# Kernel tuning notes

Measured on AMD Instinct MI355X. Metric: run time of the kernel, lower is better.

Reference implementation:

```python
import jax, jax.numpy as jnp
import numpy as np

USER = 100000
ITEM = 50000
N = USER + ITEM          # total nodes in bipartite graph
LAT = 64                 # args.latdim
TXT = 768                # args.text_feat_dim
E = 2400000              # nnz per sparse adjacency
GNN_LAYERS = 2           # args.gnn_layer
RIS_LAMBDA = 0.2         # args.ris_adj_lambda


def setup_inputs() -> dict:
    key = jax.random.key(0)
    ks = jax.random.split(key, 11)
    return {
        "uEmbeds": jax.random.normal(ks[0], (USER, LAT), jnp.float32) * 0.1,
        "iEmbeds": jax.random.normal(ks[1], (ITEM, LAT), jnp.float32) * 0.1,
        "text_embedding": jax.random.normal(ks[2], (ITEM, TXT), jnp.float32),
        "W_text": jax.random.normal(ks[3], (TXT, LAT), jnp.float32) * (1.0 / np.sqrt(TXT)),
        "b_text": jnp.zeros((LAT,), jnp.float32),
        "adj_vals": jax.random.uniform(ks[4], (E,), jnp.float32) / 16.0,
        "t_vals": jax.random.uniform(ks[5], (E,), jnp.float32) / 16.0,
        "adj_rows": jax.random.randint(ks[6], (E,), 0, N, jnp.int32),
        "adj_cols": jax.random.randint(ks[7], (E,), 0, N, jnp.int32),
        "t_rows": jax.random.randint(ks[8], (E,), 0, N, jnp.int32),
        "t_cols": jax.random.randint(ks[9], (E,), 0, N, jnp.int32),
    }


def _spmm(rows, cols, vals, x, n):
    # out[r] = sum_{e: rows[e]==r} vals[e] * x[cols[e]]  (torch.spmm on COO)
    return jax.ops.segment_sum(vals[:, None] * x[cols], rows, num_segments=n)


def _l2_normalize(x, eps=1e-12):
    # F.normalize(x, p=2, dim=1)
    nrm = jnp.sqrt(jnp.sum(x * x, axis=1, keepdims=True))
    return x / jnp.maximum(nrm, eps)


def reference(uEmbeds, iEmbeds, text_embedding, W_text, b_text,
              adj_vals, t_vals, adj_rows, adj_cols, t_rows, t_cols):
    # trans == 1: Linear projection of text features
    text_feats = text_embedding @ W_text + b_text                      # [ITEM, LAT]

    # self-propagation through text adjacency
    embeds_ta = _spmm(t_rows, t_cols, t_vals,
                      jnp.concatenate([uEmbeds, iEmbeds], axis=0), N)  # [N, LAT]

    # first hop: users + normalized text feats
    e1 = _spmm(adj_rows, adj_cols, adj_vals,
               jnp.concatenate([uEmbeds, _l2_normalize(text_feats)], axis=0), N)

    # second hop: aggregated users + raw item embeds
    e2 = _spmm(adj_rows, adj_cols, adj_vals,
               jnp.concatenate([e1[:USER], iEmbeds], axis=0), N)

    embeds = e1 + e2 + RIS_LAMBDA * embeds_ta

    # stacked GCN layers, sum of all layer outputs (incl. layer 0)
    total = embeds
    cur = embeds
    for _ in range(GNN_LAYERS):
        cur = _spmm(adj_rows, adj_cols, adj_vals, cur, N)
        total = total + cur

    return total[:USER], total[USER:]
```

## Files before the change

### kernel.cpp

```cpp
#include <hip/hip_runtime.h>

#define USER  100000
#define ITEM  50000
#define NNODE 150000
#define LAT   64
#define TXT   768
#define RP    150016
#define NBUCK 8
#define BROWS (NNODE / NBUCK)
#define SCHUNK 4096
#define CAP   64
#define GEMMB 782

typedef unsigned long long u64;

__device__ __forceinline__ void gemm_body(
    float (*As)[68], float (*Bs)[64],
    const float* __restrict__ text, const float* __restrict__ W,
    const float* __restrict__ b, float* __restrict__ tf,
    int nitems, int blk)
{
    const int tid = threadIdx.x;
    const int tx  = tid & 15;
    const int ty  = tid >> 4;
    const int row0 = blk * 64;

    float acc[4][4] = {};

    const int lrow = tid >> 3;
    const int lk4  = (tid & 7) * 4;

    for (int k0 = 0; k0 < TXT; k0 += 32) {
#pragma unroll
        for (int half = 0; half < 2; ++half) {
            int r = lrow + half * 32;
            int gr = row0 + r;
            if (gr >= nitems) gr = nitems - 1;
            float4 tv = *(const float4*)(text + (size_t)gr * TXT + k0 + lk4);
            As[lk4 + 0][r] = tv.x;
            As[lk4 + 1][r] = tv.y;
            As[lk4 + 2][r] = tv.z;
            As[lk4 + 3][r] = tv.w;
        }
        const float4* wf = (const float4*)(W + (size_t)k0 * LAT);
        ((float4*)Bs)[tid]       = wf[tid];
        ((float4*)Bs)[tid + 256] = wf[tid + 256];
        __syncthreads();

#pragma unroll
        for (int k = 0; k < 32; ++k) {
            float4 a4 = *(const float4*)&As[k][ty * 4];
            float4 b4 = *(const float4*)&Bs[k][tx * 4];
            float av[4] = {a4.x, a4.y, a4.z, a4.w};
            float bv[4] = {b4.x, b4.y, b4.z, b4.w};
#pragma unroll
            for (int i = 0; i < 4; ++i)
#pragma unroll
                for (int j = 0; j < 4; ++j)
                    acc[i][j] = fmaf(av[i], bv[j], acc[i][j]);
        }
        __syncthreads();
    }

    float4 b4 = *(const float4*)(b + tx * 4);
    float bv[4] = {b4.x, b4.y, b4.z, b4.w};
#pragma unroll
    for (int i = 0; i < 4; ++i) {
        float v[4];
        float ss = 0.f;
#pragma unroll
        for (int j = 0; j < 4; ++j) {
            v[j] = acc[i][j] + bv[j];
            ss = fmaf(v[j], v[j], ss);
        }
        ss += __shfl_xor(ss, 1);
        ss += __shfl_xor(ss, 2);
        ss += __shfl_xor(ss, 4);
        ss += __shfl_xor(ss, 8);
        float inv = 1.0f / fmaxf(sqrtf(ss), 1e-12f);
        int gr = row0 + ty * 4 + i;
        if (gr < nitems) {
            float4 o = {v[0] * inv, v[1] * inv, v[2] * inv, v[3] * inv};
            *(float4*)(tf + (size_t)gr * LAT + tx * 4) = o;
        }
    }
}

__device__ __forceinline__ void scatter_body(
    const int* __restrict__ rows, const int* __restrict__ cols,
    const float* __restrict__ vals, int* __restrict__ fil,
    u64* __restrict__ epk, int n, int bucket, int chunk)
{
    const int lo = bucket * BROWS;
    const int hi = lo + BROWS;
    const int base = chunk * SCHUNK + threadIdx.x;

    int  r[16];
    bool m[16];
    u64  pk[16];
    int  pos[16];

#pragma unroll
    for (int i = 0; i < 16; ++i) {
        int e = base + i * 256;
        bool inb = e < n;
        int rr = inb ? rows[e] : -1;
        r[i] = rr;
        m[i] = inb && (rr >= lo) && (rr < hi);
    }
#pragma unroll
    for (int i = 0; i < 16; ++i) {
        int e = base + i * 256;
        if (m[i])
            pk[i] = ((u64)__float_as_uint(vals[e]) << 32) | (unsigned)cols[e];
    }
#pragma unroll
    for (int i = 0; i < 16; ++i)
        if (m[i]) pos[i] = atomicAdd(&fil[r[i]], 1);
#pragma unroll
    for (int i = 0; i < 16; ++i)
        if (m[i] && pos[i] < CAP)
            epk[((size_t)r[i] << 6) + pos[i]] = pk[i];
}

__global__ __launch_bounds__(256) void mega1_kernel(
    const float* __restrict__ text, const float* __restrict__ W,
    const float* __restrict__ b, float* __restrict__ tf, int nitems,
    const int* __restrict__ arows, const int* __restrict__ acols,
    const float* __restrict__ avals, int* __restrict__ filA, u64* __restrict__ epkA,
    const int* __restrict__ trows, const int* __restrict__ tcols,
    const float* __restrict__ tvals, int* __restrict__ filT, u64* __restrict__ epkT,
    int nedges, int nchunk, int nscat)
{
    __shared__ float As[32][68];
    __shared__ float Bs[32][64];

    const int bid = blockIdx.x;
    const int gi  = bid / 72;
    const int pos = bid % 72;

    if (pos < 64) {
        const int so = gi * 64 + pos;
        if (so >= nscat) return;
        const int bucket = so & 7;
        const int cm     = so >> 3;
        if (cm < nchunk)
            scatter_body(arows, acols, avals, filA, epkA, nedges, bucket, cm);
        else
            scatter_body(trows, tcols, tvals, filT, epkT, nedges, bucket, cm - nchunk);
    } else {
        const int go = gi * 8 + (pos - 64);
        if (go < GEMMB)
            gemm_body(As, Bs, text, W, b, tf, nitems, go);
    }
}

__global__ __launch_bounds__(256) void gemm_norm_kernel(
    const float* __restrict__ text, const float* __restrict__ W,
    const float* __restrict__ b, float* __restrict__ tf, int nitems)
{
    __shared__ float As[32][68];
    __shared__ float Bs[32][64];
    gemm_body(As, Bs, text, W, b, tf, nitems, blockIdx.x);
}

__device__ __forceinline__ void spmm_row(
    int r, int lane, const int* __restrict__ cnt, const u64* __restrict__ epk,
    const float* __restrict__ xu, const float* __restrict__ xi,
    float scale, const float* __restrict__ add1, const float* __restrict__ add2,
    float* __restrict__ out, float* __restrict__ out2, int out2_assign)
{
    const int g = lane >> 4;
    const int l = lane & 15;

    const u64* rowp = epk + ((size_t)r << 6);
    const int deg = min(cnt[r], CAP);

    float4 acc = {0.f, 0.f, 0.f, 0.f};

    u64 pk[4];
#pragma unroll
    for (int i = 0; i < 4; ++i) pk[i] = rowp[g + i * 4];
#pragma unroll
    for (int i = 0; i < 4; ++i) {
        int ee = g + i * 4;
        if (ee < deg) {
            int   c = (int)(unsigned)(pk[i] & 0xffffffffu);
            float v = __uint_as_float((unsigned)(pk[i] >> 32));
            const float* x = (c < USER) ? (xu + (size_t)c * LAT)
                                        : (xi + (size_t)(c - USER) * LAT);
            float4 xv = *(const float4*)(x + 4 * l);
            acc.x = fmaf(v, xv.x, acc.x);
            acc.y = fmaf(v, xv.y, acc.y);
            acc.z = fmaf(v, xv.z, acc.z);
            acc.w = fmaf(v, xv.w, acc.w);
        }
    }

    if (deg > 16) {
        u64 pk2[4];
#pragma unroll
        for (int i = 0; i < 4; ++i) pk2[i] = rowp[16 + g + i * 4];
#pragma unroll
        for (int i = 0; i < 4; ++i) {
            int ee = 16 + g + i * 4;
            if (ee < deg) {
                int   c = (int)(unsigned)(pk2[i] & 0xffffffffu);
                float v = __uint_as_float((unsigned)(pk2[i] >> 32));
                const float* x = (c < USER) ? (xu + (size_t)c * LAT)
                                            : (xi + (size_t)(c - USER) * LAT);
                float4 xv = *(const float4*)(x + 4 * l);
                acc.x = fmaf(v, xv.x, acc.x);
                acc.y = fmaf(v, xv.y, acc.y);
                acc.z = fmaf(v, xv.z, acc.z);
                acc.w = fmaf(v, xv.w, acc.w);
            }
        }
        for (int ee = 32 + g; ee < deg; ee += 4) {
            u64 p = rowp[ee];
            int   c = (int)(unsigned)(p & 0xffffffffu);
            float v = __uint_as_float((unsigned)(p >> 32));
            const float* x = (c < USER) ? (xu + (size_t)c * LAT)
                                        : (xi + (size_t)(c - USER) * LAT);
            float4 xv = *(const float4*)(x + 4 * l);
            acc.x = fmaf(v, xv.x, acc.x);
            acc.y = fmaf(v, xv.y, acc.y);
            acc.z = fmaf(v, xv.z, acc.z);
            acc.w = fmaf(v, xv.w, acc.w);
        }
    }

#pragma unroll
    for (int off = 16; off <= 32; off <<= 1) {
        acc.x += __shfl_xor(acc.x, off);
        acc.y += __shfl_xor(acc.y, off);
        acc.z += __shfl_xor(acc.z, off);
        acc.w += __shfl_xor(acc.w, off);
    }
    if (g == 0) {
        size_t idx = (size_t)r * LAT + 4 * l;
        float4 res = {scale * acc.x, scale * acc.y, scale * acc.z, scale * acc.w};
        if (add1) {
            float4 a = *(const float4*)(add1 + idx);
            res.x += a.x; res.y += a.y; res.z += a.z; res.w += a.w;
        }
        if (add2) {
            float4 a = *(const float4*)(add2 + idx);
            res.x += a.x; res.y += a.y; res.z += a.z; res.w += a.w;
        }
        if (out) *(float4*)(out + idx) = res;
        if (out2) {
            if (out2_assign) {
                *(float4*)(out2 + idx) = res;
            } else {
                float4 o = *(const float4*)(out2 + idx);
                o.x += res.x; o.y += res.y; o.z += res.z; o.w += res.w;
                *(float4*)(out2 + idx) = o;
            }
        }
    }
}

__global__ __launch_bounds__(256) void spmm_kernel(
    const int* __restrict__ cnt, const u64* __restrict__ epk,
    const float* __restrict__ xu, const float* __restrict__ xi,
    float scale, const float* __restrict__ add1, const float* __restrict__ add2,
    float* __restrict__ out, float* __restrict__ out2, int out2_assign, int n)
{
    int r = blockIdx.x * 4 + (threadIdx.x >> 6);
    if (r >= n) return;
    spmm_row(r, threadIdx.x & 63, cnt, epk, xu, xi, scale,
             add1, add2, out, out2, out2_assign);
}

__global__ __launch_bounds__(256) void spmm_pair_kernel(
    const int* __restrict__ cnt0, const u64* __restrict__ epk0,
    const float* __restrict__ xu0, const float* __restrict__ xi0,
    float s0, float* __restrict__ out0,
    const int* __restrict__ cnt1, const u64* __restrict__ epk1,
    const float* __restrict__ xu1, const float* __restrict__ xi1,
    float s1, float* __restrict__ out1, int n)
{
    int m  = blockIdx.x & 1;
    int r  = (blockIdx.x >> 1) * 4 + (threadIdx.x >> 6);
    if (r >= n) return;
    int lane = threadIdx.x & 63;
    if (m == 0)
        spmm_row(r, lane, cnt0, epk0, xu0, xi0, s0, nullptr, nullptr,
                 out0, nullptr, 0);
    else
        spmm_row(r, lane, cnt1, epk1, xu1, xi1, s1, nullptr, nullptr,
                 out1, nullptr, 0);
}

__global__ __launch_bounds__(256) void spmm_atomic_kernel(
    const int* __restrict__ rows, const int* __restrict__ cols,
    const float* __restrict__ vals, float scale,
    const float* __restrict__ xu, const float* __restrict__ xi,
    float* __restrict__ out, int nedges)
{
    int e = blockIdx.x * 4 + (threadIdx.x >> 6);
    if (e >= nedges) return;
    int lane = threadIdx.x & 63;
    int r = rows[e];
    int c = cols[e];
    float v = vals[e] * scale;
    const float* x = (c < USER) ? (xu + (size_t)c * LAT)
                                : (xi + (size_t)(c - USER) * LAT);
    atomicAdd(&out[(size_t)r * LAT + lane], v * x[lane]);
}

__global__ __launch_bounds__(256) void combine_kernel(
    float* __restrict__ A, const float* __restrict__ B,
    float* __restrict__ out, int n4)
{
    int i = blockIdx.x * blockDim.x + threadIdx.x;
    if (i >= n4) return;
    float4 a = ((const float4*)A)[i];
    float4 b = ((const float4*)B)[i];
    a.x += b.x; a.y += b.y; a.z += b.z; a.w += b.w;
    ((float4*)A)[i]   = a;
    ((float4*)out)[i] = a;
}

__global__ __launch_bounds__(256) void add_kernel(
    float* __restrict__ out, const float* __restrict__ src, int n4)
{
    int i = blockIdx.x * blockDim.x + threadIdx.x;
    if (i >= n4) return;
    float4 o = ((const float4*)out)[i];
    float4 s = ((const float4*)src)[i];
    o.x += s.x; o.y += s.y; o.z += s.z; o.w += s.w;
    ((float4*)out)[i] = o;
}

extern "C" void kernel_launch(void* const* d_in, const int* in_sizes, int n_in,
                              void* d_out, int out_size, void* d_ws, size_t ws_size,
                              hipStream_t stream)
{
    const float* u        = (const float*)d_in[0];
    const float* it       = (const float*)d_in[1];
    const float* text     = (const float*)d_in[2];
    const float* W        = (const float*)d_in[3];
    const float* b        = (const float*)d_in[4];
    const float* adj_vals = (const float*)d_in[5];
    const float* t_vals   = (const float*)d_in[6];
    const int*   adj_rows = (const int*)d_in[7];
    const int*   adj_cols = (const int*)d_in[8];
    const int*   t_rows   = (const int*)d_in[9];
    const int*   t_cols   = (const int*)d_in[10];
    const int E = in_sizes[5];

    float* out = (float*)d_out;

    char* p = (char*)d_ws;
    size_t used = 0;
    auto carve = [&](size_t bytes) {
        char* q = p + used;
        used += (bytes + 255) & ~(size_t)255;
        return q;
    };
    float* A    = (float*)carve((size_t)NNODE * LAT * 4);
    float* B    = (float*)carve((size_t)NNODE * LAT * 4);
    float* tf   = (float*)carve((size_t)ITEM * LAT * 4);
    int*   filA = (int*)  carve((size_t)RP * 4);
    int*   filT = (int*)  carve((size_t)RP * 4);
    u64*   epkA = (u64*)  carve((size_t)NNODE * CAP * 8);
    u64*   epkT = (u64*)  carve((size_t)NNODE * CAP * 8);
    bool padded = (used <= ws_size);

    const int sblk   = (NNODE + 3) / 4;
    const int nchunk = (E + SCHUNK - 1) / SCHUNK;
    const int nscat  = 2 * nchunk * NBUCK;
    const int ngrp   = (nscat + 63) / 64;
    const int n4     = NNODE * LAT / 4;
    const int cblk   = (n4 + 255) / 256;

    if (padded) {
        hipMemsetAsync(filA, 0, (size_t)RP * 4 * 2, stream);
        mega1_kernel<<<ngrp * 72, 256, 0, stream>>>(
            text, W, b, tf, ITEM,
            adj_rows, adj_cols, adj_vals, filA, epkA,
            t_rows, t_cols, t_vals, filT, epkT, E, nchunk, nscat);

        spmm_pair_kernel<<<sblk * 2, 256, 0, stream>>>(
            filT, epkT, u, it, 0.2f, A,
            filA, epkA, u, tf, 1.0f, B, NNODE);

        spmm_kernel<<<sblk, 256, 0, stream>>>(filA, epkA, B, it, 1.0f,
                                              A, B, A, nullptr, 0, NNODE);
        spmm_kernel<<<sblk, 256, 0, stream>>>(filA, epkA,
                                              A, A + (size_t)USER * LAT, 1.0f,
                                              nullptr, nullptr, B, nullptr, 0, NNODE);
        spmm_kernel<<<sblk, 256, 0, stream>>>(filA, epkA,
                                              B, B + (size_t)USER * LAT, 1.0f,
                                              A, B, out, nullptr, 0, NNODE);
        return;
    }

    const size_t nbuf = (size_t)NNODE * LAT * 4;
    const int ablk = (E + 3) / 4;
    const int gblk = (ITEM + 63) / 64;
    gemm_norm_kernel<<<gblk, 256, 0, stream>>>(text, W, b, tf, ITEM);
    hipMemsetAsync(A, 0, nbuf, stream);
    hipMemsetAsync(B, 0, nbuf, stream);
    spmm_atomic_kernel<<<ablk, 256, 0, stream>>>(t_rows, t_cols, t_vals, 0.2f,
                                                 u, it, A, E);
    spmm_atomic_kernel<<<ablk, 256, 0, stream>>>(adj_rows, adj_cols, adj_vals, 1.0f,
                                                 u, tf, B, E);
    spmm_atomic_kernel<<<ablk, 256, 0, stream>>>(adj_rows, adj_cols, adj_vals, 1.0f,
                                                 B, it, A, E);
    combine_kernel<<<cblk, 256, 0, stream>>>(A, B, out, n4);
    hipMemsetAsync(B, 0, nbuf, stream);
    spmm_atomic_kernel<<<ablk, 256, 0, stream>>>(adj_rows, adj_cols, adj_vals, 1.0f,
                                                 A, A + (size_t)USER * LAT, B, E);
    add_kernel<<<cblk, 256, 0, stream>>>(out, B, n4);
    hipMemsetAsync(A, 0, nbuf, stream);
    spmm_atomic_kernel<<<ablk, 256, 0, stream>>>(adj_rows, adj_cols, adj_vals, 1.0f,
                                                 B, B + (size_t)USER * LAT, A, E);
    add_kernel<<<cblk, 256, 0, stream>>>(out, A, n4);
}
```

Baseline: 704.2 us.

## Gather SpMM operands from fp16 copies to halve random-gather traffic

Converts the user/item embeddings and the normalized text features to fp16, and has each SpMM pass also write an fp16 copy of its output for the next hop. The gathers in the CSR-bucket SpMM then read 8 bytes per lane instead of 16, while accumulation and the fp32 outputs are kept. The fp16 conversion of the inputs is folded into spare blocks of the fused scatter/GEMM kernel, and the A16 buffer reuses the epkT region once the text adjacency is consumed. The cost is reduced precision in the propagated activations, a workspace layout change, and a fallback chain if the workspace is too small.

After: 647.9 us. 8.0% less time.

```diff
diff --git a/kernel.cpp b/kernel.cpp
--- a/kernel.cpp
+++ b/kernel.cpp
@@ -1,4 +1,5 @@
 #include <hip/hip_runtime.h>
+#include <hip/hip_fp16.h>
 
 #define USER  100000
 #define ITEM  50000
@@ -14,10 +15,32 @@
 
 typedef unsigned long long u64;
 
+__device__ __forceinline__ void store4(float* p, float4 v) { *(float4*)p = v; }
+__device__ __forceinline__ void store4(__half* p, float4 v)
+{
+    __half2* d = (__half2*)p;
+    d[0] = __floats2half2_rn(v.x, v.y);
+    d[1] = __floats2half2_rn(v.z, v.w);
+}
+__device__ __forceinline__ float4 load_x4(const float* x, int l)
+{
+    return *(const float4*)(x + 4 * l);
+}
+__device__ __forceinline__ float4 load_x4(const __half* x, int l)
+{
+    float2 raw = *(const float2*)(x + 4 * l);
+    __half2 h0 = *reinterpret_cast<const __half2*>(&raw.x);
+    __half2 h1 = *reinterpret_cast<const __half2*>(&raw.y);
+    float2 f0 = __half22float2(h0);
+    float2 f1 = __half22float2(h1);
+    return make_float4(f0.x, f0.y, f1.x, f1.y);
+}
+
+template<typename TFT>
 __device__ __forceinline__ void gemm_body(
     float (*As)[68], float (*Bs)[64],
     const float* __restrict__ text, const float* __restrict__ W,
-    const float* __restrict__ b, float* __restrict__ tf,
+    const float* __restrict__ b, TFT* __restrict__ tf,
     int nitems, int blk)
 {
     const int tid = threadIdx.x;
@@ -79,10 +102,9 @@
         ss += __shfl_xor(ss, 8);
         float inv = 1.0f / fmaxf(sqrtf(ss), 1e-12f);
         int gr = row0 + ty * 4 + i;
-        if (gr < nitems) {
-            float4 o = {v[0] * inv, v[1] * inv, v[2] * inv, v[3] * inv};
-            *(float4*)(tf + (size_t)gr * LAT + tx * 4) = o;
-        }
+        if (gr < nitems)
+            store4(tf + (size_t)gr * LAT + tx * 4,
+                   make_float4(v[0] * inv, v[1] * inv, v[2] * inv, v[3] * inv));
     }
 }
 
@@ -123,14 +145,39 @@
             epk[((size_t)r[i] << 6) + pos[i]] = pk[i];
 }
 
+__device__ __forceinline__ void cvt_body(
+    const float* __restrict__ u, const float* __restrict__ it,
+    __half* __restrict__ u16, __half* __restrict__ it16,
+    int slot, int nslots)
+{
+    const long NG  = (long)NNODE * LAT / 8;
+    const long UG  = (long)USER * LAT / 8;
+    const long stride = (long)nslots * 256;
+    for (long g = (long)slot * 256 + threadIdx.x; g < NG; g += stride) {
+        const float* s; __half* d; long off;
+        if (g < UG) { s = u;  d = u16;  off = g * 8; }
+        else        { s = it; d = it16; off = (g - UG) * 8; }
+        const float4* s4 = (const float4*)(s + off);
+        float4 a = s4[0], c = s4[1];
+        __half2* d2 = (__half2*)(d + off);
+        d2[0] = __floats2half2_rn(a.x, a.y);
+        d2[1] = __floats2half2_rn(a.z, a.w);
+        d2[2] = __floats2half2_rn(c.x, c.y);
+        d2[3] = __floats2half2_rn(c.z, c.w);
+    }
+}
+
+template<typename TFT>
 __global__ __launch_bounds__(256) void mega1_kernel(
     const float* __restrict__ text, const float* __restrict__ W,
-    const float* __restrict__ b, float* __restrict__ tf, int nitems,
+    const float* __restrict__ b, TFT* __restrict__ tf, int nitems,
     const int* __restrict__ arows, const int* __restrict__ acols,
     const float* __restrict__ avals, int* __restrict__ filA, u64* __restrict__ epkA,
     const int* __restrict__ trows, const int* __restrict__ tcols,
     const float* __restrict__ tvals, int* __restrict__ filT, u64* __restrict__ epkT,
-    int nedges, int nchunk, int nscat)
+    int nedges, int nchunk, int nscat,
+    const float* __restrict__ u, const float* __restrict__ it,
+    __half* __restrict__ u16, __half* __restrict__ it16, int ncvt)
 {
     __shared__ float As[32][68];
     __shared__ float Bs[32][64];
@@ -151,7 +198,9 @@
     } else {
         const int go = gi * 8 + (pos - 64);
         if (go < GEMMB)
-            gemm_body(As, Bs, text, W, b, tf, nitems, go);
+            gemm_body<TFT>(As, Bs, text, W, b, tf, nitems, go);
+        else if (u16 && go - GEMMB < ncvt)
+            cvt_body(u, it, u16, it16, go - GEMMB, ncvt);
     }
 }
 
@@ -161,14 +210,15 @@
 {
     __shared__ float As[32][68];
     __shared__ float Bs[32][64];
-    gemm_body(As, Bs, text, W, b, tf, nitems, blockIdx.x);
-}
-
+    gemm_body<float>(As, Bs, text, W, b, tf, nitems, blockIdx.x);
+}
+
+template<typename XT>
 __device__ __forceinline__ void spmm_row(
     int r, int lane, const int* __restrict__ cnt, const u64* __restrict__ epk,
-    const float* __restrict__ xu, const float* __restrict__ xi,
+    const XT* __restrict__ xu, const XT* __restrict__ xi,
     float scale, const float* __restrict__ add1, const float* __restrict__ add2,
-    float* __restrict__ out, float* __restrict__ out2, int out2_assign)
+    float* __restrict__ out32, __half* __restrict__ out16)
 {
     const int g = lane >> 4;
     const int l = lane & 15;
@@ -187,9 +237,9 @@
         if (ee < deg) {
             int   c = (int)(unsigned)(pk[i] & 0xffffffffu);
             float v = __uint_as_float((unsigned)(pk[i] >> 32));
-            const float* x = (c < USER) ? (xu + (size_t)c * LAT)
-                                        : (xi + (size_t)(c - USER) * LAT);
-            float4 xv = *(const float4*)(x + 4 * l);
+            const XT* x = (c < USER) ? (xu + (size_t)c * LAT)
+                                     : (xi + (size_t)(c - USER) * LAT);
+            float4 xv = load_x4(x, l);
             acc.x = fmaf(v, xv.x, acc.x);
             acc.y = fmaf(v, xv.y, acc.y);
             acc.z = fmaf(v, xv.z, acc.z);
@@ -207,9 +257,9 @@
             if (ee < deg) {
                 int   c = (int)(unsigned)(pk2[i] & 0xffffffffu);
                 float v = __uint_as_float((unsigned)(pk2[i] >> 32));
-                const float* x = (c < USER) ? (xu + (size_t)c * LAT)
-                                            : (xi + (size_t)(c - USER) * LAT);
-                float4 xv = *(const float4*)(x + 4 * l);
+                const XT* x = (c < USER) ? (xu + (size_t)c * LAT)
+                                         : (xi + (size_t)(c - USER) * LAT);
+                float4 xv = load_x4(x, l);
                 acc.x = fmaf(v, xv.x, acc.x);
                 acc.y = fmaf(v, xv.y, acc.y);
                 acc.z = fmaf(v, xv.z, acc.z);
@@ -220,9 +270,9 @@
             u64 p = rowp[ee];
             int   c = (int)(unsigned)(p & 0xffffffffu);
             float v = __uint_as_float((unsigned)(p >> 32));
-            const float* x = (c < USER) ? (xu + (size_t)c * LAT)
-                                        : (xi + (size_t)(c - USER) * LAT);
-            float4 xv = *(const float4*)(x + 4 * l);
+            const XT* x = (c < USER) ? (xu + (size_t)c * LAT)
+                                     : (xi + (size_t)(c - USER) * LAT);
+            float4 xv = load_x4(x, l);
             acc.x = fmaf(v, xv.x, acc.x);
             acc.y = fmaf(v, xv.y, acc.y);
             acc.z = fmaf(v, xv.z, acc.z);
@@ -248,49 +298,43 @@
             float4 a = *(const float4*)(add2 + idx);
             res.x += a.x; res.y += a.y; res.z += a.z; res.w += a.w;
         }
-        if (out) *(float4*)(out + idx) = res;
-        if (out2) {
-            if (out2_assign) {
-                *(float4*)(out2 + idx) = res;
-            } else {
-                float4 o = *(const float4*)(out2 + idx);
-                o.x += res.x; o.y += res.y; o.z += res.z; o.w += res.w;
-                *(float4*)(out2 + idx) = o;
-            }
-        }
-    }
-}
-
+        *(float4*)(out32 + idx) = res;
+        if (out16) store4(out16 + idx, res);
+    }
+}
+
+template<typename XT>
 __global__ __launch_bounds__(256) void spmm_kernel(
     const int* __restrict__ cnt, const u64* __restrict__ epk,
-    const float* __restrict__ xu, const float* __restrict__ xi,
+    const XT* __restrict__ xu, const XT* __restrict__ xi,
     float scale, const float* __restrict__ add1, const float* __restrict__ add2,
-    float* __restrict__ out, float* __restrict__ out2, int out2_assign, int n)
+    float* __restrict__ out32, __half* __restrict__ out16, int n)
 {
     int r = blockIdx.x * 4 + (threadIdx.x >> 6);
     if (r >= n) return;
-    spmm_row(r, threadIdx.x & 63, cnt, epk, xu, xi, scale,
-             add1, add2, out, out2, out2_assign);
-}
-
+    spmm_row<XT>(r, threadIdx.x & 63, cnt, epk, xu, xi, scale,
+                 add1, add2, out32, out16);
+}
+
+template<typename XT>
 __global__ __launch_bounds__(256) void spmm_pair_kernel(
     const int* __restrict__ cnt0, const u64* __restrict__ epk0,
-    const float* __restrict__ xu0, const float* __restrict__ xi0,
-    float s0, float* __restrict__ out0,
+    const XT* __restrict__ xu0, const XT* __restrict__ xi0,
+    float s0, float* __restrict__ out0, __half* __restrict__ o16_0,
     const int* __restrict__ cnt1, const u64* __restrict__ epk1,
-    const float* __restrict__ xu1, const float* __restrict__ xi1,
-    float s1, float* __restrict__ out1, int n)
+    const XT* __restrict__ xu1, const XT* __restrict__ xi1,
+    float s1, float* __restrict__ out1, __half* __restrict__ o16_1, int n)
 {
     int m  = blockIdx.x & 1;
     int r  = (blockIdx.x >> 1) * 4 + (threadIdx.x >> 6);
     if (r >= n) return;
     int lane = threadIdx.x & 63;
     if (m == 0)
-        spmm_row(r, lane, cnt0, epk0, xu0, xi0, s0, nullptr, nullptr,
-                 out0, nullptr, 0);
+        spmm_row<XT>(r, lane, cnt0, epk0, xu0, xi0, s0, nullptr, nullptr,
+                     out0, o16_0);
     else
-        spmm_row(r, lane, cnt1, epk1, xu1, xi1, s1, nullptr, nullptr,
-                 out1, nullptr, 0);
+        spmm_row<XT>(r, lane, cnt1, epk1, xu1, xi1, s1, nullptr, nullptr,
+                     out1, o16_1);
 }
 
 __global__ __launch_bounds__(256) void spmm_atomic_kernel(
@@ -353,6 +397,14 @@
 
     float* out = (float*)d_out;
 
+    const int sblk   = (NNODE + 3) / 4;
+    const int nchunk = (E + SCHUNK - 1) / SCHUNK;
+    const int nscat  = 2 * nchunk * NBUCK;
+    const int ngrp   = (nscat + 63) / 64;
+    const int ncvt   = ngrp * 8 - GEMMB;
+    const int n4     = NNODE * LAT / 4;
+    const int cblk   = (n4 + 255) / 256;
+
     char* p = (char*)d_ws;
     size_t used = 0;
     auto carve = [&](size_t bytes) {
@@ -360,63 +412,98 @@
         used += (bytes + 255) & ~(size_t)255;
         return q;
     };
-    float* A    = (float*)carve((size_t)NNODE * LAT * 4);
-    float* B    = (float*)carve((size_t)NNODE * LAT * 4);
-    float* tf   = (float*)carve((size_t)ITEM * LAT * 4);
-    int*   filA = (int*)  carve((size_t)RP * 4);
-    int*   filT = (int*)  carve((size_t)RP * 4);
-    u64*   epkA = (u64*)  carve((size_t)NNODE * CAP * 8);
-    u64*   epkT = (u64*)  carve((size_t)NNODE * CAP * 8);
-    bool padded = (used <= ws_size);
-
-    const int sblk   = (NNODE + 3) / 4;
-    const int nchunk = (E + SCHUNK - 1) / SCHUNK;
-    const int nscat  = 2 * nchunk * NBUCK;
-    const int ngrp   = (nscat + 63) / 64;
-    const int n4     = NNODE * LAT / 4;
-    const int cblk   = (n4 + 255) / 256;
-
-    if (padded) {
+
+    used = 0;
+    float*  A    = (float*) carve((size_t)NNODE * LAT * 4);
+    float*  B    = (float*) carve((size_t)NNODE * LAT * 4);
+    int*    filA = (int*)   carve((size_t)RP * 4);
+    int*    filT = (int*)   carve((size_t)RP * 4);
+    u64*    epkA = (u64*)   carve((size_t)E ? (size_t)NNODE * CAP * 8 : 0);
+    u64*    epkT = (u64*)   carve((size_t)NNODE * CAP * 8);
+    __half* tf16 = (__half*)carve((size_t)ITEM * LAT * 2);
+    __half* u16  = (__half*)carve((size_t)NNODE * LAT * 2);
+    __half* it16 = u16 + (size_t)USER * LAT;
+    __half* B16  = (__half*)carve((size_t)NNODE * LAT * 2);
+    __half* A16  = (__half*)epkT;
+
+    if (used <= ws_size && ncvt > 0) {
         hipMemsetAsync(filA, 0, (size_t)RP * 4 * 2, stream);
-        mega1_kernel<<<ngrp * 72, 256, 0, stream>>>(
-            text, W, b, tf, ITEM,
+        mega1_kernel<__half><<<ngrp * 72, 256, 0, stream>>>(
+            text, W, b, tf16, ITEM,
             adj_rows, adj_cols, adj_vals, filA, epkA,
-            t_rows, t_cols, t_vals, filT, epkT, E, nchunk, nscat);
-
-        spmm_pair_kernel<<<sblk * 2, 256, 0, stream>>>(
-            filT, epkT, u, it, 0.2f, A,
-            filA, epkA, u, tf, 1.0f, B, NNODE);
-
-        spmm_kernel<<<sblk, 256, 0, stream>>>(filA, epkA, B, it, 1.0f,
-                                              A, B, A, nullptr, 0, NNODE);
-        spmm_kernel<<<sblk, 256, 0, stream>>>(filA, epkA,
-                                              A, A + (size_t)USER * LAT, 1.0f,
-                                              nullptr, nullptr, B, nullptr, 0, NNODE);
-        spmm_kernel<<<sblk, 256, 0, stream>>>(filA, epkA,
-                                              B, B + (size_t)USER * LAT, 1.0f,
-                                              A, B, out, nullptr, 0, NNODE);
+            t_rows, t_cols, t_vals, filT, epkT, E, nchunk, nscat,
+            u, it, u16, it16, ncvt);
+
+        spmm_pair_kernel<__half><<<sblk * 2, 256, 0, stream>>>(
+            filT, epkT, u16, it16, 0.2f, A, nullptr,
+            filA, epkA, u16, tf16, 1.0f, B, B16, NNODE);
+
+        spmm_kernel<__half><<<sblk, 256, 0, stream>>>(
+            filA, epkA, B16, it16, 1.0f, A, B, A, A16, NNODE);
+        spmm_kernel<__half><<<sblk, 256, 0, stream>>>(
+            filA, epkA, A16, A16 + (size_t)USER * LAT, 1.0f,
+            nullptr, nullptr, B, B16, NNODE);
+        spmm_kernel<__half><<<sblk, 256, 0, stream>>>(
+            filA, epkA, B16, B16 + (size_t)USER * LAT, 1.0f,
+            A, B, out, nullptr, NNODE);
         return;
     }
 
+    used = 0;
+    float* A2    = (float*)carve((size_t)NNODE * LAT * 4);
+    float* B2    = (float*)carve((size_t)NNODE * LAT * 4);
+    float* tf2   = (float*)carve((size_t)ITEM * LAT * 4);
+    int*   filA2 = (int*)  carve((size_t)RP * 4);
+    int*   filT2 = (int*)  carve((size_t)RP * 4);
+    u64*   epkA2 = (u64*)  carve((size_t)NNODE * CAP * 8);
+    u64*   epkT2 = (u64*)  carve((size_t)NNODE * CAP * 8);
+
+    if (used <= ws_size) {
+        hipMemsetAsync(filA2, 0, (size_t)RP * 4 * 2, stream);
+        mega1_kernel<float><<<ngrp * 72, 256, 0, stream>>>(
+            text, W, b, tf2, ITEM,
+            adj_rows, adj_cols, adj_vals, filA2, epkA2,
+            t_rows, t_cols, t_vals, filT2, epkT2, E, nchunk, nscat,
+            u, it, nullptr, nullptr, 0);
+
+        spmm_pair_kernel<float><<<sblk * 2, 256, 0, stream>>>(
+            filT2, epkT2, u, it, 0.2f, A2, nullptr,
+            filA2, epkA2, u, tf2, 1.0f, B2, nullptr, NNODE);
+
+        spmm_kernel<float><<<sblk, 256, 0, stream>>>(
+            filA2, epkA2, B2, it, 1.0f, A2, B2, A2, nullptr, NNODE);
+        spmm_kernel<float><<<sblk, 256, 0, stream>>>(
+            filA2, epkA2, A2, A2 + (size_t)USER * LAT, 1.0f,
+            nullptr, nullptr, B2, nullptr, NNODE);
+        spmm_kernel<float><<<sblk, 256, 0, stream>>>(
+            filA2, epkA2, B2, B2 + (size_t)USER * LAT, 1.0f,
+            A2, B2, out, nullptr, NNODE);
+        return;
+    }
+
+    used = 0;
+    float* A3  = (float*)carve((size_t)NNODE * LAT * 4);
+    float* B3  = (float*)carve((size_t)NNODE * LAT * 4);
+    float* tf3 = (float*)carve((size_t)ITEM * LAT * 4);
     const size_t nbuf = (size_t)NNODE * LAT * 4;
     const int ablk = (E + 3) / 4;
     const int gblk = (ITEM + 63) / 64;
-    gemm_norm_kernel<<<gblk, 256, 0, stream>>>(text, W, b, tf, ITEM);
-    hipMemsetAsync(A, 0, nbuf, stream);
-    hipMemsetAsync(B, 0, nbuf, stream);
+    gemm_norm_kernel<<<gblk, 256, 0, stream>>>(text, W, b, tf3, ITEM);
+    hipMemsetAsync(A3, 0, nbuf, stream);
+    hipMemsetAsync(B3, 0, nbuf, stream);
     spmm_atomic_kernel<<<ablk, 256, 0, stream>>>(t_rows, t_cols, t_vals, 0.2f,
-                                                 u, it, A, E);
+                                                 u, it, A3, E);
     spmm_atomic_kernel<<<ablk, 256, 0, stream>>>(adj_rows, adj_cols, adj_vals, 1.0f,
-                                                 u, tf, B, E);
+                                                 u, tf3, B3, E);
     spmm_atomic_kernel<<<ablk, 256, 0, stream>>>(adj_rows, adj_cols, adj_vals, 1.0f,
-                                                 B, it, A, E);
-    combine_kernel<<<cblk, 256, 0, stream>>>(A, B, out, n4);
-    hipMemsetAsync(B, 0, nbuf, stream);
+                                                 B3, it, A3, E);
+    combine_kernel<<<cblk, 256, 0, stream>>>(A3, B3, out, n4);
+    hipMemsetAsync(B3, 0, nbuf, stream);
     spmm_atomic_kernel<<<ablk, 256, 0, stream>>>(adj_rows, adj_cols, adj_vals, 1.0f,
-                                                 A, A + (size_t)USER * LAT, B, E);
-    add_kernel<<<cblk, 256, 0, stream>>>(out, B, n4);
-    hipMemsetAsync(A, 0, nbuf, stream);
+                                                 A3, A3 + (size_t)USER * LAT, B3, E);
+    add_kernel<<<cblk, 256, 0, stream>>>(out, B3, n4);
+    hipMemsetAsync(A3, 0, nbuf, stream);
     spmm_atomic_kernel<<<ablk, 256, 0, stream>>>(adj_rows, adj_cols, adj_vals, 1.0f,
-                                                 B, B + (size_t)USER * LAT, A, E);
-    add_kernel<<<cblk, 256, 0, stream>>>(out, A, n4);
-}
+                                                 B3, B3 + (size_t)USER * LAT, A3, E);
+    add_kernel<<<cblk, 256, 0, stream>>>(out, A3, n4);
+}
```
